# Kernel optimization log

Measured on AMD Instinct MI355X. Metric: run time of the kernel, lower is better.

## Reference

```python
import jax, jax.numpy as jnp
import numpy as np

STRIDE = 1
PADDING = 1


def _ternarize(w):
    # threshold = 0.75 * mean(|w|); alpha = mean(|w| over |w| > threshold)
    abs_w = jnp.abs(w)
    threshold = 0.75 * jnp.mean(abs_w)
    mask = abs_w > threshold
    cnt = jnp.sum(mask)
    alpha = jnp.where(cnt > 0, jnp.sum(jnp.where(mask, abs_w, 0.0)) / jnp.maximum(cnt, 1), 1.0)
    tern = jnp.where(w > threshold, alpha, jnp.where(w < -threshold, -alpha, 0.0))
    # straight-through estimator: forward uses tern, grad flows to w as identity
    return w + jax.lax.stop_gradient(tern - w)


def setup_inputs() -> dict:
    key = jax.random.key(0)
    k_x, k_w = jax.random.split(key)
    x = jax.random.normal(k_x, (32, 256, 56, 56), dtype=jnp.float32)
    weight = jax.random.normal(k_w, (256, 256, 3, 3), dtype=jnp.float32)
    return {"x": x, "weight": weight}


def reference(x, weight):
    tw = _ternarize(weight)
    # NCHW input, OIHW kernel
    return jax.lax.conv_general_dilated(
        x, tw,
        window_strides=(STRIDE, STRIDE),
        padding=[(PADDING, PADDING), (PADDING, PADDING)],
        dimension_numbers=("NCHW", "OIHW", "NCHW"),
    )
```

## Files before the change

kernel.cpp:

```cpp
#include <hip/hip_runtime.h>
#include <hip/hip_bf16.h>

typedef short short8 __attribute__((ext_vector_type(8)));
typedef float f32x4 __attribute__((ext_vector_type(4)));

constexpr int N_  = 32;
constexpr int C_  = 256;
constexpr int K_  = 256;
constexpr int H_  = 56;
constexpr int W_  = 56;
constexpr int HW_ = H_ * W_;
constexpr int NW_ = K_ * C_ * 9;

constexpr int TH   = 4;
constexpr int NB   = 14;
constexpr int HR   = 6, HC = 58;
constexpr int NH   = HR * HC;
constexpr int BROW = 80;
constexpr int BSZ  = NH * BROW;
constexpr int NPAIR2 = 8 * NH;
constexpr int ASTEP  = 16384;

constexpr int WS_P1 = 4, WS_P2 = 260, WS_P3 = 516;
constexpr size_t WS_WQ = 4096;
constexpr size_t WS_NEEDED = WS_WQ + (size_t)NW_ * 2;

__device__ __forceinline__ unsigned f2bf(float f) {
    unsigned u = __builtin_bit_cast(unsigned, f);
    return (u + 0x7FFFu + ((u >> 16) & 1u)) >> 16;
}

__global__ void k_abs_partial(const float* __restrict__ w, float* __restrict__ ws) {
    __shared__ float sm[4];
    float s = 0.f;
    for (int i = blockIdx.x * 256 + threadIdx.x; i < NW_; i += 256 * 256)
        s += fabsf(w[i]);
    #pragma unroll
    for (int o = 32; o > 0; o >>= 1) s += __shfl_down(s, o, 64);
    const int wid = threadIdx.x >> 6, lane = threadIdx.x & 63;
    if (lane == 0) sm[wid] = s;
    __syncthreads();
    if (threadIdx.x == 0) {
        float r = 0.f;
        for (int i = 0; i < 4; ++i) r += sm[i];
        ws[WS_P1 + blockIdx.x] = r;
    }
}

__global__ void k_masked_partial(const float* __restrict__ w, float* __restrict__ ws) {
    __shared__ float sm[4];
    float t = ws[WS_P1 + threadIdx.x];
    #pragma unroll
    for (int o = 32; o > 0; o >>= 1) t += __shfl_down(t, o, 64);
    const int wid = threadIdx.x >> 6, lane = threadIdx.x & 63;
    if (lane == 0) sm[wid] = t;
    __syncthreads();
    float total = 0.f;
    for (int i = 0; i < 4; ++i) total += sm[i];
    const float thr = 0.75f * total / (float)NW_;
    if (blockIdx.x == 0 && threadIdx.x == 0) ws[0] = total;
    __syncthreads();
    float s = 0.f, c = 0.f;
    for (int i = blockIdx.x * 256 + threadIdx.x; i < NW_; i += 256 * 256) {
        float a = fabsf(w[i]);
        if (a > thr) { s += a; c += 1.f; }
    }
    #pragma unroll
    for (int o = 32; o > 0; o >>= 1) { s += __shfl_down(s, o, 64); c += __shfl_down(c, o, 64); }
    __shared__ float sm2[8];
    if (lane == 0) { sm2[wid] = s; sm2[wid + 4] = c; }
    __syncthreads();
    if (threadIdx.x == 0) {
        float S = 0.f, C2 = 0.f;
        for (int i = 0; i < 4; ++i) { S += sm2[i]; C2 += sm2[i + 4]; }
        ws[WS_P2 + blockIdx.x] = S;
        ws[WS_P3 + blockIdx.x] = C2;
    }
}

__global__ void k_final_masked(float* __restrict__ ws) {
    __shared__ float sm[8];
    float s = ws[WS_P2 + threadIdx.x];
    float c = ws[WS_P3 + threadIdx.x];
    #pragma unroll
    for (int o = 32; o > 0; o >>= 1) { s += __shfl_down(s, o, 64); c += __shfl_down(c, o, 64); }
    const int wid = threadIdx.x >> 6, lane = threadIdx.x & 63;
    if (lane == 0) { sm[wid] = s; sm[wid + 4] = c; }
    __syncthreads();
    if (threadIdx.x == 0) {
        float S = 0.f, C2 = 0.f;
        for (int i = 0; i < 4; ++i) { S += sm[i]; C2 += sm[i + 4]; }
        ws[1] = S; ws[2] = C2;
    }
}

__device__ __forceinline__ float reduce256_all(const float* __restrict__ p, float* sm) {
    float v = threadIdx.x < 256 ? p[threadIdx.x] : 0.f;
    #pragma unroll
    for (int o = 32; o > 0; o >>= 1) v += __shfl_down(v, o, 64);
    const int wid = threadIdx.x >> 6, lane = threadIdx.x & 63;
    __syncthreads();
    if (lane == 0) sm[wid] = v;
    __syncthreads();
    float total = 0.f;
    #pragma unroll
    for (int i = 0; i < 8; ++i) total += sm[i];
    return total;
}

__global__ __launch_bounds__(512) void k_quant(const float* __restrict__ w,
                                               float* __restrict__ ws,
                                               unsigned short* __restrict__ wq) {
    __shared__ float sm[8];
    const float total = reduce256_all(ws + WS_P1, sm);
    const float msum  = reduce256_all(ws + WS_P2, sm);
    const float mcnt  = reduce256_all(ws + WS_P3, sm);
    const float thr = 0.75f * total / (float)NW_;
    const float alpha = mcnt > 0.f ? msum / fmaxf(mcnt, 1.f) : 1.0f;
    if (blockIdx.x == 0 && threadIdx.x == 0) ws[3] = alpha;
    const int i = blockIdx.x * 512 + threadIdx.x;
    if (i >= NW_) return;
    const float v = w[i];
    const unsigned short q = v > thr ? (unsigned short)0x3F80
                                     : (v < -thr ? (unsigned short)0xBF80 : (unsigned short)0);
    const int k   = i / 2304;
    const int rem = i - k * 2304;
    const int c   = rem / 9;
    const int rs  = rem - c * 9;
    const int chi = c >> 5, c5 = c & 31;
    wq[(size_t)(chi * 9 + rs) * 8192 + (k << 5) + c5] = q;
}

constexpr int RSO_[9] = {
    (0*HC+0)*BROW, (0*HC+1)*BROW, (0*HC+2)*BROW,
    (1*HC+0)*BROW, (1*HC+1)*BROW, (1*HC+2)*BROW,
    (2*HC+0)*BROW, (2*HC+1)*BROW, (2*HC+2)*BROW };

struct ConvState {
    const float* xn;
    const char*  wqc;
    char*        ldsp;
    size_t       aoff;
    int          h0, tid;
    int          bB[7];
};

__device__ __forceinline__ void load_a(short8 (&d)[4], const ConvState& st, int step) {
    const char* ap = st.wqc + (size_t)step * ASTEP + st.aoff;
    d[0] = *(const short8*)(ap);
    d[1] = *(const short8*)(ap + 1024);
    d[2] = *(const short8*)(ap + 2048);
    d[3] = *(const short8*)(ap + 3072);
}

__device__ __forceinline__ void issue_b(const ConvState& st, int c0,
                                        float (&bs)[6][4], unsigned& bmask) {
    bmask = 0;
    #pragma unroll
    for (int it = 0; it < 6; ++it) {
        const int u  = it * 512 + st.tid;
        const bool vu = u < NPAIR2;
        const int uu = vu ? u : 0;
        const int c4 = uu / NH, hidx = uu - c4 * NH;
        const int hy = hidx / HC, hx = hidx - hy * HC;
        const int h  = st.h0 - 1 + hy, w = hx - 1;
        const bool ok = vu && (unsigned)h < (unsigned)H_ && (unsigned)w < (unsigned)W_;
        const int off = ok ? ((c0 + 4 * c4) * HW_ + h * W_ + w) : 0;
        const float* p = st.xn + off;
        bs[it][0] = p[0];
        bs[it][1] = p[HW_];
        bs[it][2] = p[2 * HW_];
        bs[it][3] = p[3 * HW_];
        bmask |= (ok ? 1u : 0u) << it;
    }
}

__device__ __forceinline__ void write_b(const ConvState& st, int base,
                                        const float (&bs)[6][4], unsigned bmask) {
    #pragma unroll
    for (int it = 0; it < 6; ++it) {
        const int u = it * 512 + st.tid;
        if (u < NPAIR2) {
            const int c4 = u / NH, hidx = u - c4 * NH;
            const bool ok = (bmask >> it) & 1u;
            const float f0 = ok ? bs[it][0] : 0.f;
            const float f1 = ok ? bs[it][1] : 0.f;
            const float f2 = ok ? bs[it][2] : 0.f;
            const float f3 = ok ? bs[it][3] : 0.f;
            uint2 v;
            v.x = f2bf(f0) | (f2bf(f1) << 16);
            v.y = f2bf(f2) | (f2bf(f3) << 16);
            *(uint2*)(st.ldsp + base + hidx * BROW + c4 * 8) = v;
        }
    }
}

template <int PAR, bool LASTCH>
__device__ __forceinline__ void do_chunk(int chi, const ConvState& st,
                                         short8 (&afr)[2][4], f32x4 (&acc)[4][7],
                                         float (&bs)[6][4], unsigned& bmask) {
    const int rdbase = PAR * BSZ;
    #pragma unroll
    for (int rs = 0; rs < 9; ++rs) {
        const int cur = (PAR + rs) & 1, nxt = cur ^ 1;
        const int step = chi * 9 + rs;
        if (!(LASTCH && rs == 8))
            load_a(afr[nxt], st, step + 1);

        short8 bfr[7];
        #pragma unroll
        for (int nf = 0; nf < 7; ++nf)
            bfr[nf] = *(const short8*)(st.ldsp + rdbase + st.bB[nf] + RSO_[rs]);

        __builtin_amdgcn_s_setprio(1);
        #pragma unroll
        for (int nf = 0; nf < 7; ++nf)
            #pragma unroll
            for (int mf = 0; mf < 4; ++mf)
                acc[mf][nf] = __builtin_amdgcn_mfma_f32_16x16x32_bf16(
                    afr[cur][mf], bfr[nf], acc[mf][nf], 0, 0, 0);
        __builtin_amdgcn_s_setprio(0);

        if (rs == 6 && !LASTCH)
            issue_b(st, (chi + 1) * 32, bs, bmask);
        if (rs == 8 && !LASTCH) {
            write_b(st, (PAR ^ 1) * BSZ, bs, bmask);
            asm volatile("s_waitcnt lgkmcnt(0)" ::: "memory");
            __builtin_amdgcn_s_barrier();
        }
    }
}

__global__ __launch_bounds__(512, 2) void conv_mfma(const float* __restrict__ x,
                                                    const unsigned short* __restrict__ wq,
                                                    const float* __restrict__ wsc,
                                                    float* __restrict__ out) {
    __shared__ char lds[2 * BSZ];
    const int tid = threadIdx.x, lane = tid & 63, wid = tid >> 6;
    const int wm = wid & 3, wn = wid >> 2, lr = lane & 15, lg = lane >> 4;
    const int band = blockIdx.x, n = blockIdx.y;

    ConvState st;
    st.xn   = x + (size_t)n * C_ * HW_;
    st.wqc  = (const char*)wq;
    st.ldsp = lds;
    st.aoff = (size_t)(wm * 64 + lr) * 64 + lg * 16;
    st.h0   = band * TH;
    st.tid  = tid;
    #pragma unroll
    for (int nf = 0; nf < 7; ++nf) {
        const int pos = wn * 112 + nf * 16 + lr;
        const int y = pos / 56, xx = pos - y * 56;
        st.bB[nf] = (y * HC + xx) * BROW + lg * 16;
    }

    f32x4 acc[4][7] = {};
    short8 afr[2][4];
    float bs[6][4];
    unsigned bmask;

    issue_b(st, 0, bs, bmask);
    load_a(afr[0], st, 0);
    write_b(st, 0, bs, bmask);
    asm volatile("s_waitcnt lgkmcnt(0)" ::: "memory");
    __builtin_amdgcn_s_barrier();

    for (int cc = 0; cc < 3; ++cc) {
        do_chunk<0, false>(2 * cc,     st, afr, acc, bs, bmask);
        do_chunk<1, false>(2 * cc + 1, st, afr, acc, bs, bmask);
    }
    do_chunk<0, false>(6, st, afr, acc, bs, bmask);
    do_chunk<1, true >(7, st, afr, acc, bs, bmask);

    const float alpha = wsc[3];
    #pragma unroll
    for (int mf = 0; mf < 4; ++mf) {
        const int k = wm * 64 + mf * 16 + lg * 4;
        #pragma unroll
        for (int nf = 0; nf < 7; ++nf) {
            const int pos = wn * 112 + nf * 16 + lr;
            const int y = pos / 56, xx = pos - y * 56;
            float* po = out + ((size_t)n * K_ + k) * HW_ + (st.h0 + y) * W_ + xx;
            #pragma unroll
            for (int j = 0; j < 4; ++j)
                po[(size_t)j * HW_] = alpha * acc[mf][nf][j];
        }
    }
}

constexpr int W4_ = W_ / 4;
constexpr int SP_ = H_ * W4_;
__global__ __launch_bounds__(256) void conv_tern_otf(const float* __restrict__ x,
                                                     const float* __restrict__ wt,
                                                     const float* __restrict__ wsc,
                                                     float* __restrict__ out) {
    const int kg = blockIdx.x, n = blockIdx.y, k0 = kg * 4;
    const float thr = 0.75f * wsc[0] / (float)NW_;
    const float cnt = wsc[2];
    const float alpha = cnt > 0.f ? wsc[1] / fmaxf(cnt, 1.f) : 1.0f;
    for (int j = 0; j < 4; ++j) {
        const int sp = (int)threadIdx.x + j * 256;
        if (sp >= SP_) break;
        const int h = sp / W4_, w0 = (sp % W4_) * 4;
        float acc[4][4];
        #pragma unroll
        for (int kt = 0; kt < 4; ++kt)
            #pragma unroll
            for (int jj = 0; jj < 4; ++jj) acc[kt][jj] = 0.f;
        for (int c = 0; c < C_; ++c) {
            const float* xp = x + (((size_t)n * C_ + c) * H_) * W_;
            float xr[3][6];
            #pragma unroll
            for (int r = 0; r < 3; ++r) {
                const int hh = h + r - 1;
                const float* rowp = xp + hh * W_;
                if ((unsigned)hh < (unsigned)H_) {
                    const float4 mid = *(const float4*)(rowp + w0);
                    xr[r][1] = mid.x; xr[r][2] = mid.y; xr[r][3] = mid.z; xr[r][4] = mid.w;
                    xr[r][0] = (w0 > 0)      ? rowp[w0 - 1] : 0.f;
                    xr[r][5] = (w0 + 4 < W_) ? rowp[w0 + 4] : 0.f;
                } else {
                    #pragma unroll
                    for (int q = 0; q < 6; ++q) xr[r][q] = 0.f;
                }
            }
            #pragma unroll
            for (int kt = 0; kt < 4; ++kt) {
                const float* wp = wt + ((size_t)(k0 + kt) * C_ + c) * 9;
                #pragma unroll
                for (int r = 0; r < 3; ++r)
                    #pragma unroll
                    for (int s = 0; s < 3; ++s) {
                        float wv = wp[r * 3 + s];
                        wv = wv > thr ? alpha : (wv < -thr ? -alpha : 0.f);
                        #pragma unroll
                        for (int jj = 0; jj < 4; ++jj)
                            acc[kt][jj] = fmaf(wv, xr[r][jj + s], acc[kt][jj]);
                    }
            }
        }
        #pragma unroll
        for (int kt = 0; kt < 4; ++kt) {
            float4 o;
            o.x = acc[kt][0]; o.y = acc[kt][1]; o.z = acc[kt][2]; o.w = acc[kt][3];
            *(float4*)(out + ((((size_t)n * K_ + (k0 + kt)) * H_ + h) * W_ + w0)) = o;
        }
    }
}

extern "C" void kernel_launch(void* const* d_in, const int* in_sizes, int n_in,
                              void* d_out, int out_size, void* d_ws, size_t ws_size,
                              hipStream_t stream) {
    const float* x = (const float*)d_in[0];
    const float* w = (const float*)d_in[1];
    float* out = (float*)d_out;
    float* ws  = (float*)d_ws;
    unsigned short* wq = (unsigned short*)((char*)d_ws + WS_WQ);

    k_abs_partial<<<256, 256, 0, stream>>>(w, ws);
    k_masked_partial<<<256, 256, 0, stream>>>(w, ws);

    if (ws_size >= WS_NEEDED) {
        k_quant<<<(NW_ + 511) / 512, 512, 0, stream>>>(w, ws, wq);
        dim3 grid(NB, N_);
        conv_mfma<<<grid, 512, 0, stream>>>(x, wq, ws, out);
    } else {
        k_final_masked<<<1, 256, 0, stream>>>(ws);
        dim3 grid(64, N_);
        conv_tern_otf<<<grid, 256, 0, stream>>>(x, w, ws, out);
    }
}
```

Before: 128.9 us.

## Halve conv tile to 2-row bands with 256-thread blocks and pre-packed staging

Shrinks each block's output tile from 4 rows to 2 rows (28 bands instead of 14) and drops from 8 to 4 waves per block, so each wave covers the full 112-pixel tile. The halo input staging now converts to bf16 at global-load time and keeps packed uint2 values in registers rather than raw floats, and the s_setprio calls around the MFMA loop are removed. The goal is more blocks and occupancy with smaller LDS per block and lower register pressure for staging. In exchange the halo overhead per output row goes up (4 input rows for 2 output rows), and each block re-reads all weights for less output work.

Result: slower. 261.1 us (+102.6%).

```diff
diff --git a/kernel.cpp b/kernel.cpp
--- a/kernel.cpp
+++ b/kernel.cpp
@@ -12,13 +12,14 @@
 constexpr int HW_ = H_ * W_;
 constexpr int NW_ = K_ * C_ * 9;
 
-constexpr int TH   = 4;
-constexpr int NB   = 14;
-constexpr int HR   = 6, HC = 58;
+constexpr int TH   = 2;
+constexpr int NB   = 28;
+constexpr int HR   = 4, HC = 58;
 constexpr int NH   = HR * HC;
 constexpr int BROW = 80;
 constexpr int BSZ  = NH * BROW;
 constexpr int NPAIR2 = 8 * NH;
+constexpr int SITER  = 8;
 constexpr int ASTEP  = 16384;
 
 constexpr int WS_P1 = 4, WS_P2 = 260, WS_P3 = 516;
@@ -153,12 +154,10 @@
     d[3] = *(const short8*)(ap + 3072);
 }
 
-__device__ __forceinline__ void issue_b(const ConvState& st, int c0,
-                                        float (&bs)[6][4], unsigned& bmask) {
-    bmask = 0;
-    #pragma unroll
-    for (int it = 0; it < 6; ++it) {
-        const int u  = it * 512 + st.tid;
+__device__ __forceinline__ void issue_b(const ConvState& st, int c0, uint2 (&sv)[SITER]) {
+    #pragma unroll
+    for (int it = 0; it < SITER; ++it) {
+        const int u  = it * 256 + st.tid;
         const bool vu = u < NPAIR2;
         const int uu = vu ? u : 0;
         const int c4 = uu / NH, hidx = uu - c4 * NH;
@@ -167,30 +166,22 @@
         const bool ok = vu && (unsigned)h < (unsigned)H_ && (unsigned)w < (unsigned)W_;
         const int off = ok ? ((c0 + 4 * c4) * HW_ + h * W_ + w) : 0;
         const float* p = st.xn + off;
-        bs[it][0] = p[0];
-        bs[it][1] = p[HW_];
-        bs[it][2] = p[2 * HW_];
-        bs[it][3] = p[3 * HW_];
-        bmask |= (ok ? 1u : 0u) << it;
-    }
-}
-
-__device__ __forceinline__ void write_b(const ConvState& st, int base,
-                                        const float (&bs)[6][4], unsigned bmask) {
-    #pragma unroll
-    for (int it = 0; it < 6; ++it) {
-        const int u = it * 512 + st.tid;
+        const float f0 = ok ? p[0]        : 0.f;
+        const float f1 = ok ? p[HW_]      : 0.f;
+        const float f2 = ok ? p[2 * HW_]  : 0.f;
+        const float f3 = ok ? p[3 * HW_]  : 0.f;
+        sv[it].x = f2bf(f0) | (f2bf(f1) << 16);
+        sv[it].y = f2bf(f2) | (f2bf(f3) << 16);
+    }
+}
+
+__device__ __forceinline__ void write_b(const ConvState& st, int base, const uint2 (&sv)[SITER]) {
+    #pragma unroll
+    for (int it = 0; it < SITER; ++it) {
+        const int u = it * 256 + st.tid;
         if (u < NPAIR2) {
             const int c4 = u / NH, hidx = u - c4 * NH;
-            const bool ok = (bmask >> it) & 1u;
-            const float f0 = ok ? bs[it][0] : 0.f;
-            const float f1 = ok ? bs[it][1] : 0.f;
-            const float f2 = ok ? bs[it][2] : 0.f;
-            const float f3 = ok ? bs[it][3] : 0.f;
-            uint2 v;
-            v.x = f2bf(f0) | (f2bf(f1) << 16);
-            v.y = f2bf(f2) | (f2bf(f3) << 16);
-            *(uint2*)(st.ldsp + base + hidx * BROW + c4 * 8) = v;
+            *(uint2*)(st.ldsp + base + hidx * BROW + c4 * 8) = sv[it];
         }
     }
 }
@@ -198,7 +189,7 @@
 template <int PAR, bool LASTCH>
 __device__ __forceinline__ void do_chunk(int chi, const ConvState& st,
                                          short8 (&afr)[2][4], f32x4 (&acc)[4][7],
-                                         float (&bs)[6][4], unsigned& bmask) {
+                                         uint2 (&sv)[SITER]) {
     const int rdbase = PAR * BSZ;
     #pragma unroll
     for (int rs = 0; rs < 9; ++rs) {
@@ -212,32 +203,30 @@
         for (int nf = 0; nf < 7; ++nf)
             bfr[nf] = *(const short8*)(st.ldsp + rdbase + st.bB[nf] + RSO_[rs]);
 
-        __builtin_amdgcn_s_setprio(1);
         #pragma unroll
         for (int nf = 0; nf < 7; ++nf)
             #pragma unroll
             for (int mf = 0; mf < 4; ++mf)
                 acc[mf][nf] = __builtin_amdgcn_mfma_f32_16x16x32_bf16(
                     afr[cur][mf], bfr[nf], acc[mf][nf], 0, 0, 0);
-        __builtin_amdgcn_s_setprio(0);
 
         if (rs == 6 && !LASTCH)
-            issue_b(st, (chi + 1) * 32, bs, bmask);
+            issue_b(st, (chi + 1) * 32, sv);
         if (rs == 8 && !LASTCH) {
-            write_b(st, (PAR ^ 1) * BSZ, bs, bmask);
+            write_b(st, (PAR ^ 1) * BSZ, sv);
             asm volatile("s_waitcnt lgkmcnt(0)" ::: "memory");
             __builtin_amdgcn_s_barrier();
         }
     }
 }
 
-__global__ __launch_bounds__(512, 2) void conv_mfma(const float* __restrict__ x,
+__global__ __launch_bounds__(256, 2) void conv_mfma(const float* __restrict__ x,
                                                     const unsigned short* __restrict__ wq,
                                                     const float* __restrict__ wsc,
                                                     float* __restrict__ out) {
     __shared__ char lds[2 * BSZ];
     const int tid = threadIdx.x, lane = tid & 63, wid = tid >> 6;
-    const int wm = wid & 3, wn = wid >> 2, lr = lane & 15, lg = lane >> 4;
+    const int wm = wid, lr = lane & 15, lg = lane >> 4;
     const int band = blockIdx.x, n = blockIdx.y;
 
     ConvState st;
@@ -249,28 +238,27 @@
     st.tid  = tid;
     #pragma unroll
     for (int nf = 0; nf < 7; ++nf) {
-        const int pos = wn * 112 + nf * 16 + lr;
+        const int pos = nf * 16 + lr;
         const int y = pos / 56, xx = pos - y * 56;
         st.bB[nf] = (y * HC + xx) * BROW + lg * 16;
     }
 
     f32x4 acc[4][7] = {};
     short8 afr[2][4];
-    float bs[6][4];
-    unsigned bmask;
-
-    issue_b(st, 0, bs, bmask);
+    uint2 sv[SITER];
+
+    issue_b(st, 0, sv);
     load_a(afr[0], st, 0);
-    write_b(st, 0, bs, bmask);
+    write_b(st, 0, sv);
     asm volatile("s_waitcnt lgkmcnt(0)" ::: "memory");
     __builtin_amdgcn_s_barrier();
 
     for (int cc = 0; cc < 3; ++cc) {
-        do_chunk<0, false>(2 * cc,     st, afr, acc, bs, bmask);
-        do_chunk<1, false>(2 * cc + 1, st, afr, acc, bs, bmask);
-    }
-    do_chunk<0, false>(6, st, afr, acc, bs, bmask);
-    do_chunk<1, true >(7, st, afr, acc, bs, bmask);
+        do_chunk<0, false>(2 * cc,     st, afr, acc, sv);
+        do_chunk<1, false>(2 * cc + 1, st, afr, acc, sv);
+    }
+    do_chunk<0, false>(6, st, afr, acc, sv);
+    do_chunk<1, true >(7, st, afr, acc, sv);
 
     const float alpha = wsc[3];
     #pragma unroll
@@ -278,7 +266,7 @@
         const int k = wm * 64 + mf * 16 + lg * 4;
         #pragma unroll
         for (int nf = 0; nf < 7; ++nf) {
-            const int pos = wn * 112 + nf * 16 + lr;
+            const int pos = nf * 16 + lr;
             const int y = pos / 56, xx = pos - y * 56;
             float* po = out + ((size_t)n * K_ + k) * HW_ + (st.h0 + y) * W_ + xx;
             #pragma unroll
@@ -363,7 +351,7 @@
     if (ws_size >= WS_NEEDED) {
         k_quant<<<(NW_ + 511) / 512, 512, 0, stream>>>(w, ws, wq);
         dim3 grid(NB, N_);
-        conv_mfma<<<grid, 512, 0, stream>>>(x, wq, ws, out);
+        conv_mfma<<<grid, 256, 0, stream>>>(x, wq, ws, out);
     } else {
         k_final_masked<<<1, 256, 0, stream>>>(ws);
         dim3 grid(64, N_);
```

## Split conv tiles into half-width column blocks with 256-thread workgroups

Applied to the files above, without the earlier changes.

Each conv workgroup now covers a 4x28 output tile instead of a 4x56 band. Each workgroup uses 4 waves over K instead of 8 waves over K and spatial halves, so the grid doubles to 28x32 blocks. Smaller LDS halo buffers should allow more resident blocks and better wave occupancy. The cost is a larger halo overhead per output (30 of 58 columns loaded per half), and the weight fragments are now reloaded by twice as many blocks.

New measurement: 142.1 us. 10.2% more time.

```diff
diff --git a/kernel.cpp b/kernel.cpp
--- a/kernel.cpp
+++ b/kernel.cpp
@@ -13,12 +13,13 @@
 constexpr int NW_ = K_ * C_ * 9;
 
 constexpr int TH   = 4;
-constexpr int NB   = 14;
-constexpr int HR   = 6, HC = 58;
+constexpr int TW   = 28;
+constexpr int HR   = 6, HC = 30;
 constexpr int NH   = HR * HC;
 constexpr int BROW = 80;
 constexpr int BSZ  = NH * BROW;
 constexpr int NPAIR2 = 8 * NH;
+constexpr int SITER  = 6;
 constexpr int ASTEP  = 16384;
 
 constexpr int WS_P1 = 4, WS_P2 = 260, WS_P3 = 516;
@@ -141,7 +142,7 @@
     const char*  wqc;
     char*        ldsp;
     size_t       aoff;
-    int          h0, tid;
+    int          h0, w0, tid;
     int          bB[7];
 };
 
@@ -154,16 +155,16 @@
 }
 
 __device__ __forceinline__ void issue_b(const ConvState& st, int c0,
-                                        float (&bs)[6][4], unsigned& bmask) {
+                                        float (&bs)[SITER][4], unsigned& bmask) {
     bmask = 0;
     #pragma unroll
-    for (int it = 0; it < 6; ++it) {
-        const int u  = it * 512 + st.tid;
+    for (int it = 0; it < SITER; ++it) {
+        const int u  = it * 256 + st.tid;
         const bool vu = u < NPAIR2;
         const int uu = vu ? u : 0;
         const int c4 = uu / NH, hidx = uu - c4 * NH;
         const int hy = hidx / HC, hx = hidx - hy * HC;
-        const int h  = st.h0 - 1 + hy, w = hx - 1;
+        const int h  = st.h0 - 1 + hy, w = st.w0 - 1 + hx;
         const bool ok = vu && (unsigned)h < (unsigned)H_ && (unsigned)w < (unsigned)W_;
         const int off = ok ? ((c0 + 4 * c4) * HW_ + h * W_ + w) : 0;
         const float* p = st.xn + off;
@@ -176,10 +177,10 @@
 }
 
 __device__ __forceinline__ void write_b(const ConvState& st, int base,
-                                        const float (&bs)[6][4], unsigned bmask) {
-    #pragma unroll
-    for (int it = 0; it < 6; ++it) {
-        const int u = it * 512 + st.tid;
+                                        const float (&bs)[SITER][4], unsigned bmask) {
+    #pragma unroll
+    for (int it = 0; it < SITER; ++it) {
+        const int u = it * 256 + st.tid;
         if (u < NPAIR2) {
             const int c4 = u / NH, hidx = u - c4 * NH;
             const bool ok = (bmask >> it) & 1u;
@@ -198,7 +199,7 @@
 template <int PAR, bool LASTCH>
 __device__ __forceinline__ void do_chunk(int chi, const ConvState& st,
                                          short8 (&afr)[2][4], f32x4 (&acc)[4][7],
-                                         float (&bs)[6][4], unsigned& bmask) {
+                                         float (&bs)[SITER][4], unsigned& bmask) {
     const int rdbase = PAR * BSZ;
     #pragma unroll
     for (int rs = 0; rs < 9; ++rs) {
@@ -231,14 +232,15 @@
     }
 }
 
-__global__ __launch_bounds__(512, 2) void conv_mfma(const float* __restrict__ x,
+__global__ __launch_bounds__(256, 2) void conv_mfma(const float* __restrict__ x,
                                                     const unsigned short* __restrict__ wq,
                                                     const float* __restrict__ wsc,
                                                     float* __restrict__ out) {
     __shared__ char lds[2 * BSZ];
     const int tid = threadIdx.x, lane = tid & 63, wid = tid >> 6;
-    const int wm = wid & 3, wn = wid >> 2, lr = lane & 15, lg = lane >> 4;
-    const int band = blockIdx.x, n = blockIdx.y;
+    const int wm = wid, lr = lane & 15, lg = lane >> 4;
+    const int bx = blockIdx.x, n = blockIdx.y;
+    const int band = bx >> 1, colb = bx & 1;
 
     ConvState st;
     st.xn   = x + (size_t)n * C_ * HW_;
@@ -246,17 +248,18 @@
     st.ldsp = lds;
     st.aoff = (size_t)(wm * 64 + lr) * 64 + lg * 16;
     st.h0   = band * TH;
+    st.w0   = colb * TW;
     st.tid  = tid;
     #pragma unroll
     for (int nf = 0; nf < 7; ++nf) {
-        const int pos = wn * 112 + nf * 16 + lr;
-        const int y = pos / 56, xx = pos - y * 56;
+        const int pos = nf * 16 + lr;
+        const int y = pos / TW, xx = pos - y * TW;
         st.bB[nf] = (y * HC + xx) * BROW + lg * 16;
     }
 
     f32x4 acc[4][7] = {};
     short8 afr[2][4];
-    float bs[6][4];
+    float bs[SITER][4];
     unsigned bmask;
 
     issue_b(st, 0, bs, bmask);
@@ -278,9 +281,9 @@
         const int k = wm * 64 + mf * 16 + lg * 4;
         #pragma unroll
         for (int nf = 0; nf < 7; ++nf) {
-            const int pos = wn * 112 + nf * 16 + lr;
-            const int y = pos / 56, xx = pos - y * 56;
-            float* po = out + ((size_t)n * K_ + k) * HW_ + (st.h0 + y) * W_ + xx;
+            const int pos = nf * 16 + lr;
+            const int y = pos / TW, xx = pos - y * TW;
+            float* po = out + ((size_t)n * K_ + k) * HW_ + (st.h0 + y) * W_ + (st.w0 + xx);
             #pragma unroll
             for (int j = 0; j < 4; ++j)
                 po[(size_t)j * HW_] = alpha * acc[mf][nf][j];
@@ -362,8 +365,8 @@
 
     if (ws_size >= WS_NEEDED) {
         k_quant<<<(NW_ + 511) / 512, 512, 0, stream>>>(w, ws, wq);
-        dim3 grid(NB, N_);
-        conv_mfma<<<grid, 512, 0, stream>>>(x, wq, ws, out);
+        dim3 grid(28, N_);
+        conv_mfma<<<grid, 256, 0, stream>>>(x, wq, ws, out);
     } else {
         k_final_masked<<<1, 256, 0, stream>>>(ws);
         dim3 grid(64, N_);
```

## Double-buffer LDS B fragments and precompute staging offsets in conv MFMA loop

Applied to the files above, without the earlier changes.

B operand fragments are now double-buffered in registers: each step prefetches the next tap's LDS reads before the current MFMAs run, so LDS latency overlaps compute. At the chunk boundary the next chunk's LDS write and barrier are moved ahead of the last step so its first fragments can be prefetched. Per-thread global staging offsets and bounds masks are precomputed once instead of recomputed with divisions every chunk, and the global prefetch is issued one step earlier. The extra 7 short8 registers and the xrel array raise register pressure, which at launch_bounds(512,2) could cause spills.

Result: slower. 304.5 us (+136.2%).

```diff
diff --git a/kernel.cpp b/kernel.cpp
--- a/kernel.cpp
+++ b/kernel.cpp
@@ -19,6 +19,7 @@
 constexpr int BROW = 80;
 constexpr int BSZ  = NH * BROW;
 constexpr int NPAIR2 = 8 * NH;
+constexpr int SITER  = 6;
 constexpr int ASTEP  = 16384;
 
 constexpr int WS_P1 = 4, WS_P2 = 260, WS_P3 = 516;
@@ -141,8 +142,10 @@
     const char*  wqc;
     char*        ldsp;
     size_t       aoff;
-    int          h0, tid;
+    int          tid;
     int          bB[7];
+    int          xrel[SITER];
+    unsigned     okm;
 };
 
 __device__ __forceinline__ void load_a(short8 (&d)[4], const ConvState& st, int step) {
@@ -153,36 +156,25 @@
     d[3] = *(const short8*)(ap + 3072);
 }
 
-__device__ __forceinline__ void issue_b(const ConvState& st, int c0,
-                                        float (&bs)[6][4], unsigned& bmask) {
-    bmask = 0;
-    #pragma unroll
-    for (int it = 0; it < 6; ++it) {
-        const int u  = it * 512 + st.tid;
-        const bool vu = u < NPAIR2;
-        const int uu = vu ? u : 0;
-        const int c4 = uu / NH, hidx = uu - c4 * NH;
-        const int hy = hidx / HC, hx = hidx - hy * HC;
-        const int h  = st.h0 - 1 + hy, w = hx - 1;
-        const bool ok = vu && (unsigned)h < (unsigned)H_ && (unsigned)w < (unsigned)W_;
-        const int off = ok ? ((c0 + 4 * c4) * HW_ + h * W_ + w) : 0;
-        const float* p = st.xn + off;
+__device__ __forceinline__ void issue_b(const ConvState& st, int c0, float (&bs)[SITER][4]) {
+    #pragma unroll
+    for (int it = 0; it < SITER; ++it) {
+        const float* p = st.xn + (size_t)c0 * HW_ + st.xrel[it];
         bs[it][0] = p[0];
         bs[it][1] = p[HW_];
         bs[it][2] = p[2 * HW_];
         bs[it][3] = p[3 * HW_];
-        bmask |= (ok ? 1u : 0u) << it;
     }
 }
 
 __device__ __forceinline__ void write_b(const ConvState& st, int base,
-                                        const float (&bs)[6][4], unsigned bmask) {
-    #pragma unroll
-    for (int it = 0; it < 6; ++it) {
+                                        const float (&bs)[SITER][4]) {
+    #pragma unroll
+    for (int it = 0; it < SITER; ++it) {
         const int u = it * 512 + st.tid;
         if (u < NPAIR2) {
             const int c4 = u / NH, hidx = u - c4 * NH;
-            const bool ok = (bmask >> it) & 1u;
+            const bool ok = (st.okm >> it) & 1u;
             const float f0 = ok ? bs[it][0] : 0.f;
             const float f1 = ok ? bs[it][1] : 0.f;
             const float f2 = ok ? bs[it][2] : 0.f;
@@ -197,20 +189,31 @@
 
 template <int PAR, bool LASTCH>
 __device__ __forceinline__ void do_chunk(int chi, const ConvState& st,
-                                         short8 (&afr)[2][4], f32x4 (&acc)[4][7],
-                                         float (&bs)[6][4], unsigned& bmask) {
+                                         short8 (&afr)[2][4], short8 (&bfr)[2][7],
+                                         f32x4 (&acc)[4][7], float (&bs)[SITER][4]) {
     const int rdbase = PAR * BSZ;
+    const int wrbase = (PAR ^ 1) * BSZ;
     #pragma unroll
     for (int rs = 0; rs < 9; ++rs) {
         const int cur = (PAR + rs) & 1, nxt = cur ^ 1;
         const int step = chi * 9 + rs;
-        if (!(LASTCH && rs == 8))
+
+        if (rs == 8 && !LASTCH) {
+            write_b(st, wrbase, bs);
+            asm volatile("s_waitcnt lgkmcnt(0)" ::: "memory");
+            __builtin_amdgcn_s_barrier();
+        }
+
+        if (!(LASTCH && rs == 8)) {
             load_a(afr[nxt], st, step + 1);
-
-        short8 bfr[7];
-        #pragma unroll
-        for (int nf = 0; nf < 7; ++nf)
-            bfr[nf] = *(const short8*)(st.ldsp + rdbase + st.bB[nf] + RSO_[rs]);
+            const int nb  = (rs == 8) ? wrbase : rdbase;
+            const int nro = (rs == 8) ? RSO_[0] : RSO_[rs + 1];
+            #pragma unroll
+            for (int nf = 0; nf < 7; ++nf)
+                bfr[nxt][nf] = *(const short8*)(st.ldsp + nb + st.bB[nf] + nro);
+        }
+        if (rs == 5 && !LASTCH)
+            issue_b(st, (chi + 1) * 32, bs);
 
         __builtin_amdgcn_s_setprio(1);
         #pragma unroll
@@ -218,16 +221,8 @@
             #pragma unroll
             for (int mf = 0; mf < 4; ++mf)
                 acc[mf][nf] = __builtin_amdgcn_mfma_f32_16x16x32_bf16(
-                    afr[cur][mf], bfr[nf], acc[mf][nf], 0, 0, 0);
+                    afr[cur][mf], bfr[cur][nf], acc[mf][nf], 0, 0, 0);
         __builtin_amdgcn_s_setprio(0);
-
-        if (rs == 6 && !LASTCH)
-            issue_b(st, (chi + 1) * 32, bs, bmask);
-        if (rs == 8 && !LASTCH) {
-            write_b(st, (PAR ^ 1) * BSZ, bs, bmask);
-            asm volatile("s_waitcnt lgkmcnt(0)" ::: "memory");
-            __builtin_amdgcn_s_barrier();
-        }
     }
 }
 
@@ -239,13 +234,13 @@
     const int tid = threadIdx.x, lane = tid & 63, wid = tid >> 6;
     const int wm = wid & 3, wn = wid >> 2, lr = lane & 15, lg = lane >> 4;
     const int band = blockIdx.x, n = blockIdx.y;
+    const int h0 = band * TH;
 
     ConvState st;
     st.xn   = x + (size_t)n * C_ * HW_;
     st.wqc  = (const char*)wq;
     st.ldsp = lds;
     st.aoff = (size_t)(wm * 64 + lr) * 64 + lg * 16;
-    st.h0   = band * TH;
     st.tid  = tid;
     #pragma unroll
     for (int nf = 0; nf < 7; ++nf) {
@@ -253,24 +248,40 @@
         const int y = pos / 56, xx = pos - y * 56;
         st.bB[nf] = (y * HC + xx) * BROW + lg * 16;
     }
+    st.okm = 0;
+    #pragma unroll
+    for (int it = 0; it < SITER; ++it) {
+        const int u  = it * 512 + tid;
+        const bool vu = u < NPAIR2;
+        const int uu = vu ? u : 0;
+        const int c4 = uu / NH, hidx = uu - c4 * NH;
+        const int hy = hidx / HC, hx = hidx - hy * HC;
+        const int h = h0 - 1 + hy, w = hx - 1;
+        const bool ok = vu && (unsigned)h < (unsigned)H_ && (unsigned)w < (unsigned)W_;
+        st.xrel[it] = ok ? (4 * c4 * HW_ + h * W_ + w) : 0;
+        st.okm |= (ok ? 1u : 0u) << it;
+    }
 
     f32x4 acc[4][7] = {};
     short8 afr[2][4];
-    float bs[6][4];
-    unsigned bmask;
-
-    issue_b(st, 0, bs, bmask);
+    short8 bfr[2][7];
+    float bs[SITER][4];
+
+    issue_b(st, 0, bs);
     load_a(afr[0], st, 0);
-    write_b(st, 0, bs, bmask);
+    write_b(st, 0, bs);
     asm volatile("s_waitcnt lgkmcnt(0)" ::: "memory");
     __builtin_amdgcn_s_barrier();
+    #pragma unroll
+    for (int nf = 0; nf < 7; ++nf)
+        bfr[0][nf] = *(const short8*)(st.ldsp + st.bB[nf] + RSO_[0]);
 
     for (int cc = 0; cc < 3; ++cc) {
-        do_chunk<0, false>(2 * cc,     st, afr, acc, bs, bmask);
-        do_chunk<1, false>(2 * cc + 1, st, afr, acc, bs, bmask);
-    }
-    do_chunk<0, false>(6, st, afr, acc, bs, bmask);
-    do_chunk<1, true >(7, st, afr, acc, bs, bmask);
+        do_chunk<0, false>(2 * cc,     st, afr, bfr, acc, bs);
+        do_chunk<1, false>(2 * cc + 1, st, afr, bfr, acc, bs);
+    }
+    do_chunk<0, false>(6, st, afr, bfr, acc, bs);
+    do_chunk<1, true >(7, st, afr, bfr, acc, bs);
 
     const float alpha = wsc[3];
     #pragma unroll
@@ -280,7 +291,7 @@
         for (int nf = 0; nf < 7; ++nf) {
             const int pos = wn * 112 + nf * 16 + lr;
             const int y = pos / 56, xx = pos - y * 56;
-            float* po = out + ((size_t)n * K_ + k) * HW_ + (st.h0 + y) * W_ + xx;
+            float* po = out + ((size_t)n * K_ + k) * HW_ + (h0 + y) * W_ + xx;
             #pragma unroll
             for (int j = 0; j < 4; ++j)
                 po[(size_t)j * HW_] = alpha * acc[mf][nf][j];
```
